# Optimization experiments

Hardware: AMD Instinct MI355X
Metric: run time of the kernel (lower is better)

The kernel has to match this reference:

```python
import jax, jax.numpy as jnp
import numpy as np

T, D = 1024, 1024            # tokens, model dim
E, K = 16, 4                 # routed experts, top-k
G, TG = 4, 2                 # expert groups, limited (top) groups
INTER = 512                  # moe_inter_dim
SHARED_INTER = 2 * INTER     # n_shared_experts * moe_inter_dim
ROUTE_SCALE = 2.5
STD = 0.02


def setup_inputs() -> dict:
    key = jax.random.key(0)
    ks = jax.random.split(key, 9)
    return {
        "x": jax.random.normal(ks[0], (T, D), jnp.float32),
        "token_mask": jnp.ones((T,), jnp.bool_),
        "gate_w": jax.random.normal(ks[1], (E, D), jnp.float32) * STD,
        "gate_bias": jnp.zeros((E,), jnp.float32),  # e_score_correction_bias (zero-init)
        "gate_projs": jax.random.normal(ks[2], (E, INTER, D), jnp.float32) * STD,
        "up_projs": jax.random.normal(ks[3], (E, INTER, D), jnp.float32) * STD,
        "down_projs": jax.random.normal(ks[4], (E, D, INTER), jnp.float32) * STD,
        "shared_gate": jax.random.normal(ks[5], (SHARED_INTER, D), jnp.float32) * STD,
        "shared_up": jax.random.normal(ks[6], (SHARED_INTER, D), jnp.float32) * STD,
        "shared_down": jax.random.normal(ks[7], (D, SHARED_INTER), jnp.float32) * STD,
    }


def _route(x, gate_w, gate_bias):
    # sigmoid scoring with e_score_correction_bias + group-limited top-k (DeepSeek-V3 style)
    scores = jax.nn.sigmoid(x @ gate_w.T)                      # [T, E]
    s = (scores + gate_bias).reshape(T, G, E // G)             # bias-corrected, grouped
    group_scores = jax.lax.top_k(s, 2)[0].sum(-1)              # [T, G] sum of top-2 per group
    gidx = jax.lax.top_k(group_scores, TG)[1]                  # [T, TG]
    gmask = jax.nn.one_hot(gidx, G, dtype=s.dtype).sum(1)      # [T, G] selected-group mask
    masked = (s * gmask[:, :, None]).reshape(T, E)
    idx = jax.lax.top_k(masked, K)[1]                          # [T, K] expert indices
    w = jnp.take_along_axis(scores, idx, axis=1)               # gather original (unbiased) scores
    w = w / w.sum(-1, keepdims=True) * ROUTE_SCALE             # sigmoid renorm + route scale
    return w.astype(x.dtype), idx


def reference(x, token_mask, gate_w, gate_bias, gate_projs, up_projs,
              down_projs, shared_gate, shared_up, shared_down):
    w, idx = _route(x, gate_w, gate_bias)
    # dense combine weights [T, E]: combine[t, e] = sum_k w[t, k] * (idx[t, k] == e)
    combine = (jax.nn.one_hot(idx, E, dtype=x.dtype) * w[..., None]).sum(1)

    def body(acc, p):
        gp, up, dp, c = p                                      # per-expert SwiGLU
        inter = jax.nn.silu(x @ gp.T) * (x @ up.T)             # [T, INTER]
        return acc + c[:, None] * (inter @ dp.T), None

    routed, _ = jax.lax.scan(
        body, jnp.zeros_like(x), (gate_projs, up_projs, down_projs, combine.T))
    shared = (jax.nn.silu(x @ shared_gate.T) * (x @ shared_up.T)) @ shared_down.T
    return routed + shared
```

## Files before the change

kernel.cpp:

```cpp
#include <hip/hip_runtime.h>
#include <stdint.h>

#define TTOK 1024
#define DMODEL 1024
#define NEXP 16
#define TOPK 4
#define INTER 512
#define NSHI 1024
#define RSCALE 2.5f

typedef __bf16 bf16;
typedef __bf16 bf16x8 __attribute__((ext_vector_type(8)));
typedef __bf16 bf16x4 __attribute__((ext_vector_type(4)));
typedef float f32x4 __attribute__((ext_vector_type(4)));

#define APLANE 2064
#define BPLANE 1040

__global__ __launch_bounds__(256)
void scores_kernel(const float* __restrict__ x, const float* __restrict__ gw,
                   float* __restrict__ scores, bf16* __restrict__ xbf) {
  __shared__ float gws[16 * 1024];
  const int tid = threadIdx.x;
  const float4* gw4 = (const float4*)gw;
#pragma unroll
  for (int i0 = 0; i0 < 4096; i0 += 256) {
    const int i = i0 + tid;
    const int e = i >> 8;
    const int dq = (i & 255) << 2;
    const int dd = (dq + 4 * e) & 1023;
    ((float4*)gws)[(e << 8) + (dd >> 2)] = gw4[i];
  }
  {
    const long xb = (long)blockIdx.x * 1024;
#pragma unroll
    for (int p = 0; p < 4; ++p) {
      const long j = xb + p * 256 + tid;
      const float4 v = ((const float4*)x)[j];
      bf16x4 o;
      o.x = (bf16)v.x; o.y = (bf16)v.y; o.z = (bf16)v.z; o.w = (bf16)v.w;
      ((bf16x4*)xbf)[j] = o;
    }
  }
  __syncthreads();
  const int kq = tid >> 6;
  const int lane = tid & 63;
  const int tl = lane >> 4;
  const int e = lane & 15;
  const long token = (long)blockIdx.x * 4 + tl;
  float acc = 0.f;
  const int dbase = kq * 256;
#pragma unroll 8
  for (int i = 0; i < 256; i += 4) {
    const int d = dbase + i;
    const float4 xv = *(const float4*)&x[token * DMODEL + d];
    const float4 wv = *(const float4*)&gws[(e << 10) + ((d + 4 * e) & 1023)];
    acc += xv.x * wv.x + xv.y * wv.y + xv.z * wv.z + xv.w * wv.w;
  }
  __syncthreads();
  gws[kq * 64 + lane] = acc;
  __syncthreads();
  if (kq == 0) {
    const float s = gws[lane] + gws[64 + lane] + gws[128 + lane] + gws[192 + lane];
    scores[token * 16 + e] = s;
  }
}

__global__ __launch_bounds__(256)
void topk_kernel(const float* __restrict__ scores, const float* __restrict__ gb,
                 int* __restrict__ tokIdx, float* __restrict__ tokW,
                 int* __restrict__ counts) {
  __shared__ int h[NEXP];
  const int tid = threadIdx.x;
  if (tid < NEXP) h[tid] = 0;
  __syncthreads();
  const int t = blockIdx.x * 256 + tid;
  float sc[NEXP], s[NEXP];
#pragma unroll
  for (int e = 0; e < NEXP; ++e) {
    const float l = scores[t * NEXP + e];
    sc[e] = 1.f / (1.f + expf(-l));
    s[e] = sc[e] + gb[e];
  }
  float gsc[4];
#pragma unroll
  for (int g = 0; g < 4; ++g) {
    const float a = s[4 * g], b = s[4 * g + 1], c = s[4 * g + 2], d = s[4 * g + 3];
    gsc[g] = fmaxf(fmaxf(fmaxf(a + b, a + c), fmaxf(a + d, b + c)),
                   fmaxf(b + d, c + d));
  }
  int g0 = 0;
  for (int g = 1; g < 4; ++g) if (gsc[g] > gsc[g0]) g0 = g;
  int g1 = (g0 == 0) ? 1 : 0;
  for (int g = 0; g < 4; ++g) if (g != g0 && gsc[g] > gsc[g1]) g1 = g;
  float m[NEXP];
#pragma unroll
  for (int e = 0; e < NEXP; ++e) {
    const int g = e >> 2;
    m[e] = (g == g0 || g == g1) ? s[e] : -1.f;
  }
  int idx[TOPK]; float wv[TOPK]; float wsum = 0.f;
  for (int k = 0; k < TOPK; ++k) {
    int am = 0; float best = m[0];
    for (int e2 = 1; e2 < NEXP; ++e2)
      if (m[e2] > best) { best = m[e2]; am = e2; }
    idx[k] = am; wv[k] = sc[am]; wsum += sc[am]; m[am] = -2.f;
  }
  const float scl = RSCALE / wsum;
  for (int k = 0; k < TOPK; ++k) {
    tokIdx[t * TOPK + k] = idx[k];
    tokW[t * TOPK + k] = wv[k] * scl;
    atomicAdd(&h[idx[k]], 1);
  }
  __syncthreads();
  if (tid < NEXP) atomicAdd(&counts[tid], h[tid]);
}

__global__ void plan_kernel(const int* __restrict__ counts, int* __restrict__ offs,
                            int* __restrict__ cursors, int* __restrict__ tileE,
                            int* __restrict__ tileR, int* __restrict__ tileCnt) {
  if (threadIdx.x == 0) {
    int acc = 0;
    for (int e = 0; e < NEXP; ++e) { offs[e] = acc; cursors[e] = acc; acc += counts[e]; }
    offs[NEXP] = acc;
    int tc = 0;
    for (int e = 0; e < NEXP; ++e)
      for (int r = offs[e]; r < offs[e + 1]; r += 128) { tileE[tc] = e; tileR[tc] = r; ++tc; }
    for (int r = 0; r < TTOK; r += 128) { tileE[tc] = NEXP; tileR[tc] = r; ++tc; }
    tileCnt[0] = tc;
  }
}

__global__ __launch_bounds__(256)
void fill_kernel(const int* __restrict__ tokIdx, int* __restrict__ cursors,
                 int* __restrict__ slotTok, int* __restrict__ tokSlot) {
  __shared__ int h[NEXP], base[NEXP];
  const int tid = threadIdx.x;
  if (tid < NEXP) h[tid] = 0;
  __syncthreads();
  const int t = blockIdx.x * 256 + tid;
  int myE[TOPK], myR[TOPK];
#pragma unroll
  for (int k = 0; k < TOPK; ++k) {
    myE[k] = tokIdx[t * TOPK + k];
    myR[k] = atomicAdd(&h[myE[k]], 1);
  }
  __syncthreads();
  if (tid < NEXP) base[tid] = atomicAdd(&cursors[tid], h[tid]);
  __syncthreads();
#pragma unroll
  for (int k = 0; k < TOPK; ++k) {
    const int slot = base[myE[k]] + myR[k];
    slotTok[slot] = t;
    tokSlot[t * TOPK + k] = slot;
  }
}

__global__ __launch_bounds__(256, 2)
void gateup_gemm(const bf16* __restrict__ xbf, const int* __restrict__ slotTok,
                 const int* __restrict__ offs, const int* __restrict__ tileE,
                 const int* __restrict__ tileR, const int* __restrict__ tileCnt,
                 const float* __restrict__ Wg, const float* __restrict__ Wu,
                 const float* __restrict__ Sg, const float* __restrict__ Su,
                 bf16* __restrict__ interR, bf16* __restrict__ interS) {
  const int y = blockIdx.y;
  if (y >= tileCnt[0]) return;
  const int e = tileE[y];
  const bool shd = (e == NEXP);
  const int n0 = blockIdx.x * 64;
  if (!shd && n0 >= INTER) return;
  const int rowStart = tileR[y];
  const int rowEnd = shd ? rowStart + 128 : offs[e + 1];
  const float* wgp = shd ? Sg : Wg + (long)e * INTER * DMODEL;
  const float* wup = shd ? Su : Wu + (long)e * INTER * DMODEL;

  __shared__ __attribute__((aligned(16))) char As[8 * APLANE];
  __shared__ __attribute__((aligned(16))) char Bg[8 * BPLANE];
  __shared__ __attribute__((aligned(16))) char Bu[8 * BPLANE];
  __shared__ int tokS[128];

  const int tid = threadIdx.x;
  if (tid < 128) {
    const int r = rowStart + tid;
    tokS[tid] = shd ? r : slotTok[r < rowEnd ? r : rowStart];
  }
  __syncthreads();

  const int arw = tid >> 3;
  const int aoct = tid & 7;
  const bf16* aSrc[4];
#pragma unroll
  for (int p = 0; p < 4; ++p)
    aSrc[p] = xbf + (long)tokS[p * 32 + arw] * DMODEL + aoct * 8;

  const int bu_ = tid >> 7;
  const int u = tid & 127;
  const int brw = u >> 4;
  const int bf4 = u & 15;
  const int boct = bf4 >> 1;
  const int bhalf = bf4 & 1;
  const float* bSrc = (bu_ ? wup : wgp) + (long)n0 * DMODEL + bf4 * 4;
  char* bDst = bu_ ? Bu : Bg;

  const int lane = tid & 63;
  const int wv = tid >> 6;
  const int q = lane >> 4;
  const int l15 = lane & 15;
  const int wm = (wv >> 1) * 64;
  const int wn = (wv & 1) * 32;

  const f32x4 fz = {0.f, 0.f, 0.f, 0.f};
  f32x4 accG[4][2], accU[4][2];
#pragma unroll
  for (int i = 0; i < 4; ++i)
#pragma unroll
    for (int j = 0; j < 2; ++j) { accG[i][j] = fz; accU[i][j] = fz; }

  bf16x8 av[4];
  float4 bv[8];
#pragma unroll
  for (int p = 0; p < 4; ++p) av[p] = *(const bf16x8*)(aSrc[p]);
#pragma unroll
  for (int p = 0; p < 8; ++p)
    bv[p] = *(const float4*)(bSrc + (long)(p * 8 + brw) * DMODEL);

  for (int k0 = 0; k0 < DMODEL; k0 += 64) {
    __syncthreads();
#pragma unroll
    for (int p = 0; p < 4; ++p)
      *(bf16x8*)(As + aoct * APLANE + (p * 32 + arw) * 16) = av[p];
#pragma unroll
    for (int p = 0; p < 8; ++p) {
      bf16x4 w;
      w.x = (bf16)bv[p].x; w.y = (bf16)bv[p].y; w.z = (bf16)bv[p].z; w.w = (bf16)bv[p].w;
      *(bf16x4*)(bDst + boct * BPLANE + (p * 8 + brw) * 16 + bhalf * 8) = w;
    }
    const int kn = k0 + 64;
    if (kn < DMODEL) {
#pragma unroll
      for (int p = 0; p < 4; ++p) av[p] = *(const bf16x8*)(aSrc[p] + kn);
#pragma unroll
      for (int p = 0; p < 8; ++p)
        bv[p] = *(const float4*)(bSrc + (long)(p * 8 + brw) * DMODEL + kn);
    }
    __syncthreads();
#pragma unroll
    for (int kb = 0; kb < 2; ++kb) {
      bf16x8 aF[4];
#pragma unroll
      for (int mi = 0; mi < 4; ++mi)
        aF[mi] = *(const bf16x8*)(As + (4 * kb + q) * APLANE + (wm + 16 * mi + l15) * 16);
#pragma unroll
      for (int ni = 0; ni < 2; ++ni) {
        const int br = wn + 16 * ni + l15;
        const bf16x8 gF = *(const bf16x8*)(Bg + (4 * kb + q) * BPLANE + br * 16);
        const bf16x8 uF = *(const bf16x8*)(Bu + (4 * kb + q) * BPLANE + br * 16);
#pragma unroll
        for (int mi = 0; mi < 4; ++mi) {
          accG[mi][ni] = __builtin_amdgcn_mfma_f32_16x16x32_bf16(aF[mi], gF, accG[mi][ni], 0, 0, 0);
          accU[mi][ni] = __builtin_amdgcn_mfma_f32_16x16x32_bf16(aF[mi], uF, accU[mi][ni], 0, 0, 0);
        }
      }
    }
  }

  bf16* outI = shd ? interS : interR;
  const int ldI = shd ? NSHI : INTER;
#pragma unroll
  for (int mi = 0; mi < 4; ++mi)
#pragma unroll
    for (int r = 0; r < 4; ++r) {
      const int rowLoc = wm + 16 * mi + q * 4 + r;
      const int row = rowStart + rowLoc;
      if (row < rowEnd) {
#pragma unroll
        for (int ni = 0; ni < 2; ++ni) {
          const float gg = accG[mi][ni][r];
          const float uu = accU[mi][ni][r];
          const float sv = gg / (1.f + __expf(-gg)) * uu;
          outI[(long)row * ldI + (n0 + wn + 16 * ni + l15)] = (bf16)sv;
        }
      }
    }
}

__global__ __launch_bounds__(256, 2)
void down_gemm(const bf16* __restrict__ interR, const bf16* __restrict__ interS,
               const int* __restrict__ offs, const int* __restrict__ tileE,
               const int* __restrict__ tileR, const int* __restrict__ tileCnt,
               const float* __restrict__ Wd, const float* __restrict__ Sd,
               float* __restrict__ dsR, float* __restrict__ dsS) {
  const int y = blockIdx.y;
  if (y >= tileCnt[0]) return;
  const int e = tileE[y];
  const bool shd = (e == NEXP);
  const int n0 = blockIdx.x * 64;
  const int rowStart = tileR[y];
  const int rowEnd = shd ? rowStart + 128 : offs[e + 1];
  const int Kd = shd ? NSHI : INTER;
  const bf16* A = shd ? interS : interR;
  const float* wd = shd ? Sd : Wd + (long)e * DMODEL * INTER;

  __shared__ __attribute__((aligned(16))) char As[8 * APLANE];
  __shared__ __attribute__((aligned(16))) char Bs[8 * BPLANE];

  const int tid = threadIdx.x;
  const int arw = tid >> 3;
  const int aoct = tid & 7;
  const bf16* aSrc[4];
#pragma unroll
  for (int p = 0; p < 4; ++p)
    aSrc[p] = A + (long)(rowStart + p * 32 + arw) * Kd + aoct * 8;

  const int brw = tid >> 4;
  const int bf4 = tid & 15;
  const int boct = bf4 >> 1;
  const int bhalf = bf4 & 1;
  const float* bSrc = wd + (long)n0 * Kd + bf4 * 4;

  const int lane = tid & 63;
  const int wv = tid >> 6;
  const int q = lane >> 4;
  const int l15 = lane & 15;
  const int wm = (wv >> 1) * 64;
  const int wn = (wv & 1) * 32;

  const f32x4 fz = {0.f, 0.f, 0.f, 0.f};
  f32x4 acc[4][2];
#pragma unroll
  for (int i = 0; i < 4; ++i)
#pragma unroll
    for (int j = 0; j < 2; ++j) acc[i][j] = fz;

  bf16x8 av[4];
  float4 bv[4];
#pragma unroll
  for (int p = 0; p < 4; ++p) av[p] = *(const bf16x8*)(aSrc[p]);
#pragma unroll
  for (int p = 0; p < 4; ++p)
    bv[p] = *(const float4*)(bSrc + (long)(p * 16 + brw) * Kd);

  for (int k0 = 0; k0 < Kd; k0 += 64) {
    __syncthreads();
#pragma unroll
    for (int p = 0; p < 4; ++p)
      *(bf16x8*)(As + aoct * APLANE + (p * 32 + arw) * 16) = av[p];
#pragma unroll
    for (int p = 0; p < 4; ++p) {
      bf16x4 w;
      w.x = (bf16)bv[p].x; w.y = (bf16)bv[p].y; w.z = (bf16)bv[p].z; w.w = (bf16)bv[p].w;
      *(bf16x4*)(Bs + boct * BPLANE + (p * 16 + brw) * 16 + bhalf * 8) = w;
    }
    const int kn = k0 + 64;
    if (kn < Kd) {
#pragma unroll
      for (int p = 0; p < 4; ++p) av[p] = *(const bf16x8*)(aSrc[p] + kn);
#pragma unroll
      for (int p = 0; p < 4; ++p)
        bv[p] = *(const float4*)(bSrc + (long)(p * 16 + brw) * Kd + kn);
    }
    __syncthreads();
#pragma unroll
    for (int kb = 0; kb < 2; ++kb) {
      bf16x8 aF[4];
#pragma unroll
      for (int mi = 0; mi < 4; ++mi)
        aF[mi] = *(const bf16x8*)(As + (4 * kb + q) * APLANE + (wm + 16 * mi + l15) * 16);
#pragma unroll
      for (int ni = 0; ni < 2; ++ni) {
        const bf16x8 bF = *(const bf16x8*)(Bs + (4 * kb + q) * BPLANE + (wn + 16 * ni + l15) * 16);
#pragma unroll
        for (int mi = 0; mi < 4; ++mi)
          acc[mi][ni] = __builtin_amdgcn_mfma_f32_16x16x32_bf16(aF[mi], bF, acc[mi][ni], 0, 0, 0);
      }
    }
  }

  float* dst = shd ? dsS : dsR;
#pragma unroll
  for (int mi = 0; mi < 4; ++mi)
#pragma unroll
    for (int r = 0; r < 4; ++r) {
      const int rowLoc = wm + 16 * mi + q * 4 + r;
      const int row = rowStart + rowLoc;
      if (row < rowEnd) {
#pragma unroll
        for (int ni = 0; ni < 2; ++ni)
          dst[(long)row * DMODEL + (n0 + wn + 16 * ni + l15)] = acc[mi][ni][r];
      }
    }
}

__global__ __launch_bounds__(256)
void combine_kernel(const float* __restrict__ dsR, const float* __restrict__ dsS,
                    const int* __restrict__ tokSlot, const float* __restrict__ tokW,
                    float* __restrict__ out) {
  const int t = blockIdx.x;
  const int j = threadIdx.x;
  float4 v = ((const float4*)(dsS + (long)t * DMODEL))[j];
#pragma unroll
  for (int k = 0; k < TOPK; ++k) {
    const int s = tokSlot[t * TOPK + k];
    const float w = tokW[t * TOPK + k];
    const float4 r = ((const float4*)(dsR + (long)s * DMODEL))[j];
    v.x += w * r.x; v.y += w * r.y; v.z += w * r.z; v.w += w * r.w;
  }
  ((float4*)(out + (long)t * DMODEL))[j] = v;
}

extern "C" void kernel_launch(void* const* d_in, const int* in_sizes, int n_in,
                              void* d_out, int out_size, void* d_ws, size_t ws_size,
                              hipStream_t stream) {
  const float* x  = (const float*)d_in[0];
  const float* gw = (const float*)d_in[2];
  const float* gb = (const float*)d_in[3];
  const float* gp = (const float*)d_in[4];
  const float* up = (const float*)d_in[5];
  const float* dp = (const float*)d_in[6];
  const float* sg = (const float*)d_in[7];
  const float* su = (const float*)d_in[8];
  const float* sd = (const float*)d_in[9];
  float* out = (float*)d_out;

  char* base = (char*)d_ws;
  size_t off = 0;
  auto alloc = [&](size_t bytes) -> char* {
    off = (off + 255) & ~(size_t)255;
    char* p = base + off;
    off += bytes;
    return p;
  };
  bf16* xbf = (bf16*)alloc((size_t)TTOK * DMODEL * 2);
  bf16* interR = (bf16*)alloc((size_t)(TTOK * TOPK + 128) * INTER * 2);
  bf16* interS = (bf16*)alloc((size_t)TTOK * NSHI * 2);
  float* dsR = (float*)alloc((size_t)TTOK * TOPK * DMODEL * 4);
  float* dsS = (float*)alloc((size_t)TTOK * DMODEL * 4);
  float* scores = (float*)alloc((size_t)TTOK * NEXP * 4);
  int* tokIdx = (int*)alloc(TTOK * TOPK * 4);
  float* tokW = (float*)alloc(TTOK * TOPK * 4);
  int* slotTok = (int*)alloc(TTOK * TOPK * 4);
  int* tokSlot = (int*)alloc(TTOK * TOPK * 4);
  int* counts = (int*)alloc(NEXP * 4);
  int* offs = (int*)alloc((NEXP + 1) * 4);
  int* cursors = (int*)alloc(NEXP * 4);
  int* tileE = (int*)alloc(72 * 4);
  int* tileR = (int*)alloc(72 * 4);
  int* tileCnt = (int*)alloc(4);

  hipMemsetAsync(counts, 0, NEXP * 4, stream);

  scores_kernel<<<TTOK / 4, 256, 0, stream>>>(x, gw, scores, xbf);
  topk_kernel<<<TTOK / 256, 256, 0, stream>>>(scores, gb, tokIdx, tokW, counts);
  plan_kernel<<<1, 64, 0, stream>>>(counts, offs, cursors, tileE, tileR, tileCnt);
  fill_kernel<<<TTOK / 256, 256, 0, stream>>>(tokIdx, cursors, slotTok, tokSlot);

  gateup_gemm<<<dim3(16, 56, 1), 256, 0, stream>>>(
      xbf, slotTok, offs, tileE, tileR, tileCnt, gp, up, sg, su, interR, interS);
  down_gemm<<<dim3(16, 56, 1), 256, 0, stream>>>(
      interR, interS, offs, tileE, tileR, tileCnt, dp, sd, dsR, dsS);
  combine_kernel<<<TTOK, 256, 0, stream>>>(dsR, dsS, tokSlot, tokW, out);
}
```

Before: 220.7 us.

## Fuse routing into one block kernel and halve GEMM N-tile width

Replaces the topk, plan and fill kernels plus the memset with a single 1024-thread route_kernel that does top-k, counting, tile planning and slot assignment in shared memory. This removes three launches and the global atomics between them. Both expert GEMMs now use 32-column N tiles with 4 warps stacked along M, which doubles the grid to give more blocks for occupancy but lowers per-block reuse. Barriers are replaced with an lgkmcnt wait plus s_barrier.

```diff
diff --git a/kernel.cpp b/kernel.cpp
--- a/kernel.cpp
+++ b/kernel.cpp
@@ -15,7 +15,13 @@
 typedef float f32x4 __attribute__((ext_vector_type(4)));
 
 #define APLANE 2064
-#define BPLANE 1040
+#define BPLANE 528
+
+#define LGKM_BAR()                                            \
+  do {                                                        \
+    asm volatile("s_waitcnt lgkmcnt(0)" ::: "memory");        \
+    __builtin_amdgcn_s_barrier();                             \
+  } while (0)
 
 __global__ __launch_bounds__(256)
 void scores_kernel(const float* __restrict__ x, const float* __restrict__ gw,
@@ -66,15 +72,16 @@
   }
 }
 
-__global__ __launch_bounds__(256)
-void topk_kernel(const float* __restrict__ scores, const float* __restrict__ gb,
-                 int* __restrict__ tokIdx, float* __restrict__ tokW,
-                 int* __restrict__ counts) {
-  __shared__ int h[NEXP];
-  const int tid = threadIdx.x;
-  if (tid < NEXP) h[tid] = 0;
-  __syncthreads();
-  const int t = blockIdx.x * 256 + tid;
+__global__ __launch_bounds__(1024)
+void route_kernel(const float* __restrict__ scores, const float* __restrict__ gb,
+                  float* __restrict__ tokW, int* __restrict__ slotTok,
+                  int* __restrict__ tokSlot, int* __restrict__ offs,
+                  int* __restrict__ tileE, int* __restrict__ tileR,
+                  int* __restrict__ tileCnt) {
+  __shared__ int cnt[NEXP], cur[NEXP];
+  const int t = threadIdx.x;
+  if (t < NEXP) cnt[t] = 0;
+  __syncthreads();
   float sc[NEXP], s[NEXP];
 #pragma unroll
   for (int e = 0; e < NEXP; ++e) {
@@ -106,53 +113,34 @@
       if (m[e2] > best) { best = m[e2]; am = e2; }
     idx[k] = am; wv[k] = sc[am]; wsum += sc[am]; m[am] = -2.f;
   }
-  const float scl = RSCALE / wsum;
-  for (int k = 0; k < TOPK; ++k) {
-    tokIdx[t * TOPK + k] = idx[k];
-    tokW[t * TOPK + k] = wv[k] * scl;
-    atomicAdd(&h[idx[k]], 1);
-  }
-  __syncthreads();
-  if (tid < NEXP) atomicAdd(&counts[tid], h[tid]);
-}
-
-__global__ void plan_kernel(const int* __restrict__ counts, int* __restrict__ offs,
-                            int* __restrict__ cursors, int* __restrict__ tileE,
-                            int* __restrict__ tileR, int* __restrict__ tileCnt) {
-  if (threadIdx.x == 0) {
+#pragma unroll
+  for (int k = 0; k < TOPK; ++k) atomicAdd(&cnt[idx[k]], 1);
+  __syncthreads();
+  if (t == 0) {
     int acc = 0;
-    for (int e = 0; e < NEXP; ++e) { offs[e] = acc; cursors[e] = acc; acc += counts[e]; }
+#pragma unroll
+    for (int e = 0; e < NEXP; ++e) {
+      offs[e] = acc; cur[e] = acc; acc += cnt[e];
+    }
     offs[NEXP] = acc;
     int tc = 0;
-    for (int e = 0; e < NEXP; ++e)
-      for (int r = offs[e]; r < offs[e + 1]; r += 128) { tileE[tc] = e; tileR[tc] = r; ++tc; }
+    int roff = 0;
+    for (int e = 0; e < NEXP; ++e) {
+      const int end = roff + cnt[e];
+      for (int r = roff; r < end; r += 128) { tileE[tc] = e; tileR[tc] = r; ++tc; }
+      roff = end;
+    }
     for (int r = 0; r < TTOK; r += 128) { tileE[tc] = NEXP; tileR[tc] = r; ++tc; }
     tileCnt[0] = tc;
   }
-}
-
-__global__ __launch_bounds__(256)
-void fill_kernel(const int* __restrict__ tokIdx, int* __restrict__ cursors,
-                 int* __restrict__ slotTok, int* __restrict__ tokSlot) {
-  __shared__ int h[NEXP], base[NEXP];
-  const int tid = threadIdx.x;
-  if (tid < NEXP) h[tid] = 0;
-  __syncthreads();
-  const int t = blockIdx.x * 256 + tid;
-  int myE[TOPK], myR[TOPK];
+  __syncthreads();
+  const float scl = RSCALE / wsum;
 #pragma unroll
   for (int k = 0; k < TOPK; ++k) {
-    myE[k] = tokIdx[t * TOPK + k];
-    myR[k] = atomicAdd(&h[myE[k]], 1);
-  }
-  __syncthreads();
-  if (tid < NEXP) base[tid] = atomicAdd(&cursors[tid], h[tid]);
-  __syncthreads();
-#pragma unroll
-  for (int k = 0; k < TOPK; ++k) {
-    const int slot = base[myE[k]] + myR[k];
+    const int slot = atomicAdd(&cur[idx[k]], 1);
     slotTok[slot] = t;
     tokSlot[t * TOPK + k] = slot;
+    tokW[t * TOPK + k] = wv[k] * scl;
   }
 }
 
@@ -167,7 +155,7 @@
   if (y >= tileCnt[0]) return;
   const int e = tileE[y];
   const bool shd = (e == NEXP);
-  const int n0 = blockIdx.x * 64;
+  const int n0 = blockIdx.x * 32;
   if (!shd && n0 >= INTER) return;
   const int rowStart = tileR[y];
   const int rowEnd = shd ? rowStart + 128 : offs[e + 1];
@@ -206,31 +194,30 @@
   const int wv = tid >> 6;
   const int q = lane >> 4;
   const int l15 = lane & 15;
-  const int wm = (wv >> 1) * 64;
-  const int wn = (wv & 1) * 32;
+  const int wm = wv * 32;
 
   const f32x4 fz = {0.f, 0.f, 0.f, 0.f};
-  f32x4 accG[4][2], accU[4][2];
-#pragma unroll
-  for (int i = 0; i < 4; ++i)
+  f32x4 accG[2][2], accU[2][2];
+#pragma unroll
+  for (int i = 0; i < 2; ++i)
 #pragma unroll
     for (int j = 0; j < 2; ++j) { accG[i][j] = fz; accU[i][j] = fz; }
 
   bf16x8 av[4];
-  float4 bv[8];
+  float4 bv[4];
 #pragma unroll
   for (int p = 0; p < 4; ++p) av[p] = *(const bf16x8*)(aSrc[p]);
 #pragma unroll
-  for (int p = 0; p < 8; ++p)
+  for (int p = 0; p < 4; ++p)
     bv[p] = *(const float4*)(bSrc + (long)(p * 8 + brw) * DMODEL);
 
   for (int k0 = 0; k0 < DMODEL; k0 += 64) {
-    __syncthreads();
+    LGKM_BAR();
 #pragma unroll
     for (int p = 0; p < 4; ++p)
       *(bf16x8*)(As + aoct * APLANE + (p * 32 + arw) * 16) = av[p];
 #pragma unroll
-    for (int p = 0; p < 8; ++p) {
+    for (int p = 0; p < 4; ++p) {
       bf16x4 w;
       w.x = (bf16)bv[p].x; w.y = (bf16)bv[p].y; w.z = (bf16)bv[p].z; w.w = (bf16)bv[p].w;
       *(bf16x4*)(bDst + boct * BPLANE + (p * 8 + brw) * 16 + bhalf * 8) = w;
@@ -240,23 +227,23 @@
 #pragma unroll
       for (int p = 0; p < 4; ++p) av[p] = *(const bf16x8*)(aSrc[p] + kn);
 #pragma unroll
-      for (int p = 0; p < 8; ++p)
+      for (int p = 0; p < 4; ++p)
         bv[p] = *(const float4*)(bSrc + (long)(p * 8 + brw) * DMODEL + kn);
     }
-    __syncthreads();
+    LGKM_BAR();
 #pragma unroll
     for (int kb = 0; kb < 2; ++kb) {
-      bf16x8 aF[4];
-#pragma unroll
-      for (int mi = 0; mi < 4; ++mi)
+      bf16x8 aF[2];
+#pragma unroll
+      for (int mi = 0; mi < 2; ++mi)
         aF[mi] = *(const bf16x8*)(As + (4 * kb + q) * APLANE + (wm + 16 * mi + l15) * 16);
 #pragma unroll
       for (int ni = 0; ni < 2; ++ni) {
-        const int br = wn + 16 * ni + l15;
+        const int br = 16 * ni + l15;
         const bf16x8 gF = *(const bf16x8*)(Bg + (4 * kb + q) * BPLANE + br * 16);
         const bf16x8 uF = *(const bf16x8*)(Bu + (4 * kb + q) * BPLANE + br * 16);
 #pragma unroll
-        for (int mi = 0; mi < 4; ++mi) {
+        for (int mi = 0; mi < 2; ++mi) {
           accG[mi][ni] = __builtin_amdgcn_mfma_f32_16x16x32_bf16(aF[mi], gF, accG[mi][ni], 0, 0, 0);
           accU[mi][ni] = __builtin_amdgcn_mfma_f32_16x16x32_bf16(aF[mi], uF, accU[mi][ni], 0, 0, 0);
         }
@@ -267,7 +254,7 @@
   bf16* outI = shd ? interS : interR;
   const int ldI = shd ? NSHI : INTER;
 #pragma unroll
-  for (int mi = 0; mi < 4; ++mi)
+  for (int mi = 0; mi < 2; ++mi)
 #pragma unroll
     for (int r = 0; r < 4; ++r) {
       const int rowLoc = wm + 16 * mi + q * 4 + r;
@@ -278,7 +265,7 @@
           const float gg = accG[mi][ni][r];
           const float uu = accU[mi][ni][r];
           const float sv = gg / (1.f + __expf(-gg)) * uu;
-          outI[(long)row * ldI + (n0 + wn + 16 * ni + l15)] = (bf16)sv;
+          outI[(long)row * ldI + (n0 + 16 * ni + l15)] = (bf16)sv;
         }
       }
     }
@@ -294,7 +281,7 @@
   if (y >= tileCnt[0]) return;
   const int e = tileE[y];
   const bool shd = (e == NEXP);
-  const int n0 = blockIdx.x * 64;
+  const int n0 = blockIdx.x * 32;
   const int rowStart = tileR[y];
   const int rowEnd = shd ? rowStart + 128 : offs[e + 1];
   const int Kd = shd ? NSHI : INTER;
@@ -322,31 +309,30 @@
   const int wv = tid >> 6;
   const int q = lane >> 4;
   const int l15 = lane & 15;
-  const int wm = (wv >> 1) * 64;
-  const int wn = (wv & 1) * 32;
+  const int wm = wv * 32;
 
   const f32x4 fz = {0.f, 0.f, 0.f, 0.f};
-  f32x4 acc[4][2];
-#pragma unroll
-  for (int i = 0; i < 4; ++i)
+  f32x4 acc[2][2];
+#pragma unroll
+  for (int i = 0; i < 2; ++i)
 #pragma unroll
     for (int j = 0; j < 2; ++j) acc[i][j] = fz;
 
   bf16x8 av[4];
-  float4 bv[4];
+  float4 bv[2];
 #pragma unroll
   for (int p = 0; p < 4; ++p) av[p] = *(const bf16x8*)(aSrc[p]);
 #pragma unroll
-  for (int p = 0; p < 4; ++p)
+  for (int p = 0; p < 2; ++p)
     bv[p] = *(const float4*)(bSrc + (long)(p * 16 + brw) * Kd);
 
   for (int k0 = 0; k0 < Kd; k0 += 64) {
-    __syncthreads();
+    LGKM_BAR();
 #pragma unroll
     for (int p = 0; p < 4; ++p)
       *(bf16x8*)(As + aoct * APLANE + (p * 32 + arw) * 16) = av[p];
 #pragma unroll
-    for (int p = 0; p < 4; ++p) {
+    for (int p = 0; p < 2; ++p) {
       bf16x4 w;
       w.x = (bf16)bv[p].x; w.y = (bf16)bv[p].y; w.z = (bf16)bv[p].z; w.w = (bf16)bv[p].w;
       *(bf16x4*)(Bs + boct * BPLANE + (p * 16 + brw) * 16 + bhalf * 8) = w;
@@ -356,21 +342,21 @@
 #pragma unroll
       for (int p = 0; p < 4; ++p) av[p] = *(const bf16x8*)(aSrc[p] + kn);
 #pragma unroll
-      for (int p = 0; p < 4; ++p)
+      for (int p = 0; p < 2; ++p)
         bv[p] = *(const float4*)(bSrc + (long)(p * 16 + brw) * Kd + kn);
     }
-    __syncthreads();
+    LGKM_BAR();
 #pragma unroll
     for (int kb = 0; kb < 2; ++kb) {
-      bf16x8 aF[4];
-#pragma unroll
-      for (int mi = 0; mi < 4; ++mi)
+      bf16x8 aF[2];
+#pragma unroll
+      for (int mi = 0; mi < 2; ++mi)
         aF[mi] = *(const bf16x8*)(As + (4 * kb + q) * APLANE + (wm + 16 * mi + l15) * 16);
 #pragma unroll
       for (int ni = 0; ni < 2; ++ni) {
-        const bf16x8 bF = *(const bf16x8*)(Bs + (4 * kb + q) * BPLANE + (wn + 16 * ni + l15) * 16);
-#pragma unroll
-        for (int mi = 0; mi < 4; ++mi)
+        const bf16x8 bF = *(const bf16x8*)(Bs + (4 * kb + q) * BPLANE + (16 * ni + l15) * 16);
+#pragma unroll
+        for (int mi = 0; mi < 2; ++mi)
           acc[mi][ni] = __builtin_amdgcn_mfma_f32_16x16x32_bf16(aF[mi], bF, acc[mi][ni], 0, 0, 0);
       }
     }
@@ -378,7 +364,7 @@
 
   float* dst = shd ? dsS : dsR;
 #pragma unroll
-  for (int mi = 0; mi < 4; ++mi)
+  for (int mi = 0; mi < 2; ++mi)
 #pragma unroll
     for (int r = 0; r < 4; ++r) {
       const int rowLoc = wm + 16 * mi + q * 4 + r;
@@ -386,7 +372,7 @@
       if (row < rowEnd) {
 #pragma unroll
         for (int ni = 0; ni < 2; ++ni)
-          dst[(long)row * DMODEL + (n0 + wn + 16 * ni + l15)] = acc[mi][ni][r];
+          dst[(long)row * DMODEL + (n0 + 16 * ni + l15)] = acc[mi][ni][r];
       }
     }
 }
@@ -436,27 +422,21 @@
   float* dsR = (float*)alloc((size_t)TTOK * TOPK * DMODEL * 4);
   float* dsS = (float*)alloc((size_t)TTOK * DMODEL * 4);
   float* scores = (float*)alloc((size_t)TTOK * NEXP * 4);
-  int* tokIdx = (int*)alloc(TTOK * TOPK * 4);
   float* tokW = (float*)alloc(TTOK * TOPK * 4);
   int* slotTok = (int*)alloc(TTOK * TOPK * 4);
   int* tokSlot = (int*)alloc(TTOK * TOPK * 4);
-  int* counts = (int*)alloc(NEXP * 4);
   int* offs = (int*)alloc((NEXP + 1) * 4);
-  int* cursors = (int*)alloc(NEXP * 4);
   int* tileE = (int*)alloc(72 * 4);
   int* tileR = (int*)alloc(72 * 4);
   int* tileCnt = (int*)alloc(4);
 
-  hipMemsetAsync(counts, 0, NEXP * 4, stream);
-
   scores_kernel<<<TTOK / 4, 256, 0, stream>>>(x, gw, scores, xbf);
-  topk_kernel<<<TTOK / 256, 256, 0, stream>>>(scores, gb, tokIdx, tokW, counts);
-  plan_kernel<<<1, 64, 0, stream>>>(counts, offs, cursors, tileE, tileR, tileCnt);
-  fill_kernel<<<TTOK / 256, 256, 0, stream>>>(tokIdx, cursors, slotTok, tokSlot);
-
-  gateup_gemm<<<dim3(16, 56, 1), 256, 0, stream>>>(
+  route_kernel<<<1, 1024, 0, stream>>>(scores, gb, tokW, slotTok, tokSlot,
+                                       offs, tileE, tileR, tileCnt);
+
+  gateup_gemm<<<dim3(32, 56, 1), 256, 0, stream>>>(
       xbf, slotTok, offs, tileE, tileR, tileCnt, gp, up, sg, su, interR, interS);
-  down_gemm<<<dim3(16, 56, 1), 256, 0, stream>>>(
+  down_gemm<<<dim3(32, 56, 1), 256, 0, stream>>>(
       interR, interS, offs, tileE, tileR, tileCnt, dp, sd, dsR, dsS);
   combine_kernel<<<TTOK, 256, 0, stream>>>(dsR, dsS, tokSlot, tokW, out);
 }
```

Result: slower. 231.6 us (+4.9%).
